# Kernel tuning notes

Hardware: AMD Instinct MI355X
Metric: run time of the kernel (lower is better)

The kernel has to match this reference:

```python
import jax, jax.numpy as jnp
import numpy as np

N_NODES = 50000
N_EDGES = 800000
IN_CH = 128
HID = 128


def setup_inputs() -> dict:
    key = jax.random.key(0)
    ks = jax.random.split(key, 16)
    inp = {
        "x": jax.random.normal(ks[0], (N_NODES, IN_CH), dtype=jnp.float32),
        "edge_index": jax.random.randint(ks[1], (2, N_EDGES), 0, N_NODES, dtype=jnp.int64),
        "batch_size": 1024,
    }
    dims = [(IN_CH, HID), (HID, HID), (HID, HID)]
    for i, (din, dout) in enumerate(dims):
        s = 1.0 / np.sqrt(din)
        inp[f"W_l{i}"] = jax.random.uniform(ks[2 + 4 * i], (dout, din), jnp.float32, -s, s)
        inp[f"b_l{i}"] = jax.random.uniform(ks[3 + 4 * i], (dout,), jnp.float32, -s, s)
        inp[f"W_r{i}"] = jax.random.uniform(ks[4 + 4 * i], (dout, din), jnp.float32, -s, s)
        inp[f"a{i}"] = jnp.full((dout,), 0.25, dtype=jnp.float32)  # PReLU slope
    return inp


def _sage_prelu(x, src, dst, W_l, b_l, W_r, a):
    # mean aggregation of source messages at target nodes
    msg_sum = jax.ops.segment_sum(x[src], dst, num_segments=N_NODES)  # [N, din]
    deg = jax.ops.segment_sum(jnp.ones((src.shape[0],), x.dtype), dst, num_segments=N_NODES)
    agg = msg_sum / jnp.maximum(deg, 1.0)[:, None]
    out = agg @ W_l.T + b_l + x @ W_r.T  # lin_l(aggr) + lin_r(x), bias on lin_l only
    return jnp.where(out > 0, out, a * out)  # per-channel PReLU


def reference(x, edge_index, batch_size, W_l0, b_l0, W_r0, a0, W_l1, b_l1, W_r1, a1, W_l2, b_l2, W_r2, a2):
    src, dst = edge_index[0], edge_index[1]
    x = _sage_prelu(x, src, dst, W_l0, b_l0, W_r0, a0)
    x = _sage_prelu(x, src, dst, W_l1, b_l1, W_r1, a1)
    x = _sage_prelu(x, src, dst, W_l2, b_l2, W_r2, a2)
    return x[:batch_size]
```

## Files before the change

kernel.cpp:

```cpp
#include <hip/hip_runtime.h>

#define NN 50000
#define NE 800000
#define C 128
#define SCAN_BLOCKS ((NN + 255) / 256)
#define ASTRIDE 136

typedef __attribute__((ext_vector_type(8))) short bf16x8;
typedef __attribute__((ext_vector_type(4))) float f32x4;
typedef unsigned short ushort;

__device__ inline ushort bf16_rn(float f) {
    unsigned u = __builtin_bit_cast(unsigned, f);
    u += 0x7FFF + ((u >> 16) & 1);
    return (ushort)(u >> 16);
}
__device__ inline void split_bf16(float f, ushort& hi, ushort& lo) {
    hi = bf16_rn(f);
    float hif = __builtin_bit_cast(float, (unsigned)hi << 16);
    lo = bf16_rn(f - hif);
}
__device__ inline float bf_lo(unsigned u) { return __builtin_bit_cast(float, u << 16); }
__device__ inline float bf_hi(unsigned u) { return __builtin_bit_cast(float, u & 0xFFFF0000u); }


__global__ __launch_bounds__(256)
void count_pos_kernel(const int* __restrict__ dst, int* __restrict__ deg,
                      int* __restrict__ pos, int n_edges) {
    int e0 = (blockIdx.x * 256 + threadIdx.x) * 8;
    if (e0 >= n_edges) return;
    int4 a = *(const int4*)(dst + e0);
    int4 b = *(const int4*)(dst + e0 + 4);
    int p0 = atomicAdd(&deg[a.x], 1);
    int p1 = atomicAdd(&deg[a.y], 1);
    int p2 = atomicAdd(&deg[a.z], 1);
    int p3 = atomicAdd(&deg[a.w], 1);
    int p4 = atomicAdd(&deg[b.x], 1);
    int p5 = atomicAdd(&deg[b.y], 1);
    int p6 = atomicAdd(&deg[b.z], 1);
    int p7 = atomicAdd(&deg[b.w], 1);
    *(int4*)(pos + e0)     = make_int4(p0, p1, p2, p3);
    *(int4*)(pos + e0 + 4) = make_int4(p4, p5, p6, p7);
}

__global__ __launch_bounds__(256)
void scan1_kernel(const int* __restrict__ deg, int* __restrict__ row_ptr,
                  int* __restrict__ bsum, int n) {
    __shared__ int wsum[4];
    __shared__ int wpre[4];
    int t = threadIdx.x, lane = t & 63, w = t >> 6;
    int i = blockIdx.x * 256 + t;
    int v = (i < n) ? deg[i] : 0;
    int s = v;
    #pragma unroll
    for (int off = 1; off < 64; off <<= 1) {
        int y = __shfl_up(s, off, 64);
        if (lane >= off) s += y;
    }
    if (lane == 63) wsum[w] = s;
    __syncthreads();
    if (t == 0) {
        int acc = 0;
        #pragma unroll
        for (int j = 0; j < 4; ++j) { wpre[j] = acc; acc += wsum[j]; }
        bsum[blockIdx.x] = acc;
    }
    __syncthreads();
    if (i < n) row_ptr[i] = wpre[w] + (s - v);
}

__global__ __launch_bounds__(256)
void scan2_kernel(const int* __restrict__ bsum, int* __restrict__ boff,
                  int* __restrict__ row_ptr, int nb, int n) {
    __shared__ int wsum[4];
    __shared__ int wpre[4];
    int t = threadIdx.x, lane = t & 63, w = t >> 6;
    int v = (t < nb) ? bsum[t] : 0;
    int s = v;
    #pragma unroll
    for (int off = 1; off < 64; off <<= 1) {
        int y = __shfl_up(s, off, 64);
        if (lane >= off) s += y;
    }
    if (lane == 63) wsum[w] = s;
    __syncthreads();
    if (t == 0) {
        int acc = 0;
        #pragma unroll
        for (int j = 0; j < 4; ++j) { wpre[j] = acc; acc += wsum[j]; }
        row_ptr[n] = acc;
    }
    __syncthreads();
    if (t < nb) boff[t] = wpre[w] + (s - v);
}

__global__ __launch_bounds__(256)
void scan3_kernel(int* __restrict__ row_ptr, const int* __restrict__ boff, int n) {
    int i = blockIdx.x * 256 + threadIdx.x;
    if (i < n) row_ptr[i] += boff[blockIdx.x];
}


__global__ __launch_bounds__(256)
void fill2_kernel(const int* __restrict__ src, const int* __restrict__ dst,
                  const int* __restrict__ row_ptr, const int* __restrict__ pos,
                  int* __restrict__ col, int n_edges) {
    int e0 = (blockIdx.x * 256 + threadIdx.x) * 8;
    if (e0 >= n_edges) return;
    int4 da = *(const int4*)(dst + e0);
    int4 db = *(const int4*)(dst + e0 + 4);
    int4 sa = *(const int4*)(src + e0);
    int4 sb = *(const int4*)(src + e0 + 4);
    int4 pa = *(const int4*)(pos + e0);
    int4 pb = *(const int4*)(pos + e0 + 4);
    col[row_ptr[da.x] + pa.x] = sa.x;
    col[row_ptr[da.y] + pa.y] = sa.y;
    col[row_ptr[da.z] + pa.z] = sa.z;
    col[row_ptr[da.w] + pa.w] = sa.w;
    col[row_ptr[db.x] + pb.x] = sb.x;
    col[row_ptr[db.y] + pb.y] = sb.y;
    col[row_ptr[db.z] + pb.z] = sb.z;
    col[row_ptr[db.w] + pb.w] = sb.w;
}


__global__ __launch_bounds__(256)
void split_kernel(const float* __restrict__ in, ushort* __restrict__ h,
                  ushort* __restrict__ l, int n4) {
    int i = blockIdx.x * 256 + threadIdx.x;
    if (i >= n4) return;
    f32x4 v = ((const f32x4*)in)[i];
    ushort h0, h1, h2, h3, l0, l1, l2, l3;
    split_bf16(v.x, h0, l0);
    split_bf16(v.y, h1, l1);
    split_bf16(v.z, h2, l2);
    split_bf16(v.w, h3, l3);
    *(uint2*)(h + i * 4) = make_uint2((unsigned)h0 | ((unsigned)h1 << 16),
                                      (unsigned)h2 | ((unsigned)h3 << 16));
    *(uint2*)(l + i * 4) = make_uint2((unsigned)l0 | ((unsigned)l1 << 16),
                                      (unsigned)l2 | ((unsigned)l3 << 16));
}


__global__ __launch_bounds__(256)
void agg_kernel(const ushort* __restrict__ xh, const int* __restrict__ row_ptr,
                const int* __restrict__ col, float* __restrict__ agg, int nodes) {
    int node = (blockIdx.x * blockDim.x + threadIdx.x) >> 6;
    int lane = threadIdx.x & 63;
    if (node >= nodes) return;
    int quad = lane >> 4;
    int ql   = lane & 15;
    int start = row_ptr[node], end = row_ptr[node + 1];
    const uint4* xr = (const uint4*)xh;
    float a0=0,a1=0,a2=0,a3=0,a4=0,a5=0,a6=0,a7=0;
    int e = start;
    for (; e + 7 < end; e += 8) {
        int i0 = col[e + quad];
        int i1 = col[e + 4 + quad];
        uint4 u0 = xr[(size_t)i0 * 16 + ql];
        uint4 u1 = xr[(size_t)i1 * 16 + ql];
        a0 += bf_lo(u0.x) + bf_lo(u1.x); a1 += bf_hi(u0.x) + bf_hi(u1.x);
        a2 += bf_lo(u0.y) + bf_lo(u1.y); a3 += bf_hi(u0.y) + bf_hi(u1.y);
        a4 += bf_lo(u0.z) + bf_lo(u1.z); a5 += bf_hi(u0.z) + bf_hi(u1.z);
        a6 += bf_lo(u0.w) + bf_lo(u1.w); a7 += bf_hi(u0.w) + bf_hi(u1.w);
    }
    for (; e + 3 < end; e += 4) {
        uint4 u = xr[(size_t)col[e + quad] * 16 + ql];
        a0 += bf_lo(u.x); a1 += bf_hi(u.x);
        a2 += bf_lo(u.y); a3 += bf_hi(u.y);
        a4 += bf_lo(u.z); a5 += bf_hi(u.z);
        a6 += bf_lo(u.w); a7 += bf_hi(u.w);
    }
    int rem = end - e;
    if (quad < rem) {
        uint4 u = xr[(size_t)col[e + quad] * 16 + ql];
        a0 += bf_lo(u.x); a1 += bf_hi(u.x);
        a2 += bf_lo(u.y); a3 += bf_hi(u.y);
        a4 += bf_lo(u.z); a5 += bf_hi(u.z);
        a6 += bf_lo(u.w); a7 += bf_hi(u.w);
    }
    a0 += __shfl_xor(a0, 16, 64); a0 += __shfl_xor(a0, 32, 64);
    a1 += __shfl_xor(a1, 16, 64); a1 += __shfl_xor(a1, 32, 64);
    a2 += __shfl_xor(a2, 16, 64); a2 += __shfl_xor(a2, 32, 64);
    a3 += __shfl_xor(a3, 16, 64); a3 += __shfl_xor(a3, 32, 64);
    a4 += __shfl_xor(a4, 16, 64); a4 += __shfl_xor(a4, 32, 64);
    a5 += __shfl_xor(a5, 16, 64); a5 += __shfl_xor(a5, 32, 64);
    a6 += __shfl_xor(a6, 16, 64); a6 += __shfl_xor(a6, 32, 64);
    a7 += __shfl_xor(a7, 16, 64); a7 += __shfl_xor(a7, 32, 64);
    if (quad == 0) {
        float inv = 1.0f / (float)max(end - start, 1);
        float* dst = agg + (size_t)node * C + ql * 8;
        *(f32x4*)dst       = (f32x4){a0 * inv, a1 * inv, a2 * inv, a3 * inv};
        *(f32x4*)(dst + 4) = (f32x4){a4 * inv, a5 * inv, a6 * inv, a7 * inv};
    }
}


__global__ __launch_bounds__(256, 3)
void gemm_kernel(const float* __restrict__ Ain,
                 const ushort* __restrict__ Xh, const ushort* __restrict__ Xl,
                 const float* __restrict__ Wl, const float* __restrict__ bl,
                 const float* __restrict__ Wr, const float* __restrict__ slope,
                 float* __restrict__ outf, ushort* __restrict__ outh,
                 ushort* __restrict__ outl, int rows) {
    __shared__ ushort Ahi[64 * ASTRIDE];
    __shared__ ushort Alo[64 * ASTRIDE];
    int t = threadIdx.x;
    int lane = t & 63;
    int w = t >> 6;
    int l = lane & 15;
    int q = lane >> 4;
    int row0 = blockIdx.x * 64;

    f32x4 acc[4][2];
    #pragma unroll
    for (int mt = 0; mt < 4; ++mt)
        #pragma unroll
        for (int nt = 0; nt < 2; ++nt)
            acc[mt][nt] = (f32x4){0.f, 0.f, 0.f, 0.f};

    #pragma unroll
    for (int mat = 0; mat < 2; ++mat) {
        const float* W = mat ? Wr : Wl;

        bf16x8 bhi[2][4], blo[2][4];
        #pragma unroll
        for (int nt = 0; nt < 2; ++nt) {
            int n = w * 32 + nt * 16 + l;
            const float* wp = W + n * C + q * 8;
            #pragma unroll
            for (int kb = 0; kb < 4; ++kb) {
                f32x4 w0 = *(const f32x4*)(wp + kb * 32);
                f32x4 w1 = *(const f32x4*)(wp + kb * 32 + 4);
                float f[8] = {w0.x, w0.y, w0.z, w0.w, w1.x, w1.y, w1.z, w1.w};
                bf16x8 h, o;
                #pragma unroll
                for (int j = 0; j < 8; ++j) {
                    ushort hh, ll;
                    split_bf16(f[j], hh, ll);
                    h[j] = (short)hh;
                    o[j] = (short)ll;
                }
                bhi[nt][kb] = h;
                blo[nt][kb] = o;
            }
        }

        __syncthreads();
        int ar = t >> 2;
        int aq = t & 3;
        int r = min(row0 + ar, rows - 1);
        ushort* dh = Ahi + ar * ASTRIDE + aq * 32;
        ushort* dl = Alo + ar * ASTRIDE + aq * 32;
        if (mat == 0) {
            const float* ap = Ain + (size_t)r * C + aq * 32;
            #pragma unroll
            for (int i = 0; i < 8; ++i) {
                f32x4 v = *(const f32x4*)(ap + i * 4);
                ushort h0, h1, h2, h3, l0, l1, l2, l3;
                split_bf16(v.x, h0, l0);
                split_bf16(v.y, h1, l1);
                split_bf16(v.z, h2, l2);
                split_bf16(v.w, h3, l3);
                *(uint2*)(dh + i * 4) = make_uint2((unsigned)h0 | ((unsigned)h1 << 16),
                                                   (unsigned)h2 | ((unsigned)h3 << 16));
                *(uint2*)(dl + i * 4) = make_uint2((unsigned)l0 | ((unsigned)l1 << 16),
                                                   (unsigned)l2 | ((unsigned)l3 << 16));
            }
        } else {
            const ushort* ph = Xh + (size_t)r * C + aq * 32;
            const ushort* pl = Xl + (size_t)r * C + aq * 32;
            #pragma unroll
            for (int i = 0; i < 4; ++i) {
                *(uint4*)(dh + i * 8) = *(const uint4*)(ph + i * 8);
                *(uint4*)(dl + i * 8) = *(const uint4*)(pl + i * 8);
            }
        }
        __syncthreads();

        #pragma unroll
        for (int kb = 0; kb < 4; ++kb) {
            #pragma unroll
            for (int mt = 0; mt < 4; ++mt) {
                int off = (mt * 16 + l) * ASTRIDE + kb * 32 + q * 8;
                bf16x8 ahi = *(const bf16x8*)(Ahi + off);
                bf16x8 alo = *(const bf16x8*)(Alo + off);
                #pragma unroll
                for (int nt = 0; nt < 2; ++nt) {
                    acc[mt][nt] = __builtin_amdgcn_mfma_f32_16x16x32_bf16(ahi, bhi[nt][kb], acc[mt][nt], 0, 0, 0);
                    acc[mt][nt] = __builtin_amdgcn_mfma_f32_16x16x32_bf16(alo, bhi[nt][kb], acc[mt][nt], 0, 0, 0);
                    acc[mt][nt] = __builtin_amdgcn_mfma_f32_16x16x32_bf16(ahi, blo[nt][kb], acc[mt][nt], 0, 0, 0);
                }
            }
        }
    }

    #pragma unroll
    for (int nt = 0; nt < 2; ++nt) {
        int n = w * 32 + nt * 16 + l;
        float b = bl[n], s = slope[n];
        #pragma unroll
        for (int mt = 0; mt < 4; ++mt) {
            #pragma unroll
            for (int rg = 0; rg < 4; ++rg) {
                int r = row0 + mt * 16 + q * 4 + rg;
                if (r < rows) {
                    float v = acc[mt][nt][rg] + b;
                    v = v > 0.f ? v : s * v;
                    if (outf) {
                        outf[(size_t)r * C + n] = v;
                    } else {
                        ushort hh, ll;
                        split_bf16(v, hh, ll);
                        outh[(size_t)r * C + n] = hh;
                        outl[(size_t)r * C + n] = ll;
                    }
                }
            }
        }
    }
}


extern "C" void kernel_launch(void* const* d_in, const int* in_sizes, int n_in,
                              void* d_out, int out_size, void* d_ws, size_t ws_size,
                              hipStream_t stream) {
    const float* x   = (const float*)d_in[0];
    const int*   src = (const int*)d_in[1];
    const int*   dst = src + NE;
    const float* Wl[3] = {(const float*)d_in[3], (const float*)d_in[7],  (const float*)d_in[11]};
    const float* bl[3] = {(const float*)d_in[4], (const float*)d_in[8],  (const float*)d_in[12]};
    const float* Wr[3] = {(const float*)d_in[5], (const float*)d_in[9],  (const float*)d_in[13]};
    const float* sl[3] = {(const float*)d_in[6], (const float*)d_in[10], (const float*)d_in[14]};

    int*   deg     = (int*)d_ws;
    int*   row_ptr = deg + 50016;
    int*   col     = row_ptr + 50016;
    int*   pos     = col + 800000;
    int*   bsum    = pos + 800000;
    int*   boff    = bsum + 256;
    float* agg     = (float*)(boff + 256);
    ushort* Ah     = (ushort*)(agg + (size_t)NN * C);
    ushort* Al     = Ah + (size_t)NN * C;
    ushort* Bh     = Al + (size_t)NN * C;
    ushort* Bl     = Bh + (size_t)NN * C;

    hipMemsetAsync(deg, 0, 50016 * sizeof(int), stream);

    const int E8B = (NE / 8 + 255) / 256;
    count_pos_kernel<<<E8B, 256, 0, stream>>>(dst, deg, pos, NE);
    scan1_kernel<<<SCAN_BLOCKS, 256, 0, stream>>>(deg, row_ptr, bsum, NN);
    scan2_kernel<<<1, 256, 0, stream>>>(bsum, boff, row_ptr, SCAN_BLOCKS, NN);
    scan3_kernel<<<SCAN_BLOCKS, 256, 0, stream>>>(row_ptr, boff, NN);
    fill2_kernel<<<E8B, 256, 0, stream>>>(src, dst, row_ptr, pos, col, NE);

    split_kernel<<<(NN * C / 4 + 255) / 256, 256, 0, stream>>>(x, Ah, Al, NN * C / 4);

    int rows_out = out_size / C;

    agg_kernel<<<(NN + 3) / 4, 256, 0, stream>>>(Ah, row_ptr, col, agg, NN);
    gemm_kernel<<<(NN + 63) / 64, 256, 0, stream>>>(agg, Ah, Al, Wl[0], bl[0], Wr[0], sl[0],
                                                    nullptr, Bh, Bl, NN);

    agg_kernel<<<(NN + 3) / 4, 256, 0, stream>>>(Bh, row_ptr, col, agg, NN);
    gemm_kernel<<<(NN + 63) / 64, 256, 0, stream>>>(agg, Bh, Bl, Wl[1], bl[1], Wr[1], sl[1],
                                                    nullptr, Ah, Al, NN);

    agg_kernel<<<(rows_out + 3) / 4, 256, 0, stream>>>(Ah, row_ptr, col, agg, rows_out);
    gemm_kernel<<<(rows_out + 63) / 64, 256, 0, stream>>>(agg, Ah, Al, Wl[2], bl[2], Wr[2], sl[2],
                                                          (float*)d_out, nullptr, nullptr, rows_out);
}
```

Before: 310.5 us.

## Fuse CSR build and bf16 split into one cooperative kernel with grid syncs

Replaces the memset, count, three scan, fill and split kernel launches with a single cooperative kernel that separates phases with grid-wide syncs. The bf16 hi/lo split of x is folded into the degree-counting phase as a grid-stride loop. This is meant to remove per-launch overhead and inter-kernel gaps for the small preprocessing steps. In exchange it adds grid.sync costs, and it depends on all 391 blocks being co-resident, which the cooperative launch requires.

```diff
diff --git a/kernel.cpp b/kernel.cpp
--- a/kernel.cpp
+++ b/kernel.cpp
@@ -1,9 +1,13 @@
 #include <hip/hip_runtime.h>
+#include <hip/hip_cooperative_groups.h>
+
+namespace cg = cooperative_groups;
 
 #define NN 50000
 #define NE 800000
 #define C 128
 #define SCAN_BLOCKS ((NN + 255) / 256)
+#define PRE_BLOCKS (NE / (256 * 8))
 #define ASTRIDE 136
 
 typedef __attribute__((ext_vector_type(8))) short bf16x8;
@@ -25,120 +29,121 @@
 
 
 __global__ __launch_bounds__(256)
-void count_pos_kernel(const int* __restrict__ dst, int* __restrict__ deg,
-                      int* __restrict__ pos, int n_edges) {
-    int e0 = (blockIdx.x * 256 + threadIdx.x) * 8;
-    if (e0 >= n_edges) return;
-    int4 a = *(const int4*)(dst + e0);
-    int4 b = *(const int4*)(dst + e0 + 4);
-    int p0 = atomicAdd(&deg[a.x], 1);
-    int p1 = atomicAdd(&deg[a.y], 1);
-    int p2 = atomicAdd(&deg[a.z], 1);
-    int p3 = atomicAdd(&deg[a.w], 1);
-    int p4 = atomicAdd(&deg[b.x], 1);
-    int p5 = atomicAdd(&deg[b.y], 1);
-    int p6 = atomicAdd(&deg[b.z], 1);
-    int p7 = atomicAdd(&deg[b.w], 1);
-    *(int4*)(pos + e0)     = make_int4(p0, p1, p2, p3);
-    *(int4*)(pos + e0 + 4) = make_int4(p4, p5, p6, p7);
-}
-
-__global__ __launch_bounds__(256)
-void scan1_kernel(const int* __restrict__ deg, int* __restrict__ row_ptr,
-                  int* __restrict__ bsum, int n) {
+void preproc_kernel(const int* __restrict__ src, const int* __restrict__ dst,
+                    const float* __restrict__ x,
+                    int* __restrict__ deg, int* __restrict__ row_ptr,
+                    int* __restrict__ pos, int* __restrict__ col,
+                    int* __restrict__ bsum, int* __restrict__ boff,
+                    ushort* __restrict__ Ah, ushort* __restrict__ Al) {
+    cg::grid_group grid = cg::this_grid();
     __shared__ int wsum[4];
     __shared__ int wpre[4];
     int t = threadIdx.x, lane = t & 63, w = t >> 6;
-    int i = blockIdx.x * 256 + t;
-    int v = (i < n) ? deg[i] : 0;
-    int s = v;
-    #pragma unroll
-    for (int off = 1; off < 64; off <<= 1) {
-        int y = __shfl_up(s, off, 64);
-        if (lane >= off) s += y;
-    }
-    if (lane == 63) wsum[w] = s;
-    __syncthreads();
-    if (t == 0) {
-        int acc = 0;
-        #pragma unroll
-        for (int j = 0; j < 4; ++j) { wpre[j] = acc; acc += wsum[j]; }
-        bsum[blockIdx.x] = acc;
-    }
-    __syncthreads();
-    if (i < n) row_ptr[i] = wpre[w] + (s - v);
-}
-
-__global__ __launch_bounds__(256)
-void scan2_kernel(const int* __restrict__ bsum, int* __restrict__ boff,
-                  int* __restrict__ row_ptr, int nb, int n) {
-    __shared__ int wsum[4];
-    __shared__ int wpre[4];
-    int t = threadIdx.x, lane = t & 63, w = t >> 6;
-    int v = (t < nb) ? bsum[t] : 0;
-    int s = v;
-    #pragma unroll
-    for (int off = 1; off < 64; off <<= 1) {
-        int y = __shfl_up(s, off, 64);
-        if (lane >= off) s += y;
-    }
-    if (lane == 63) wsum[w] = s;
-    __syncthreads();
-    if (t == 0) {
-        int acc = 0;
-        #pragma unroll
-        for (int j = 0; j < 4; ++j) { wpre[j] = acc; acc += wsum[j]; }
-        row_ptr[n] = acc;
-    }
-    __syncthreads();
-    if (t < nb) boff[t] = wpre[w] + (s - v);
-}
-
-__global__ __launch_bounds__(256)
-void scan3_kernel(int* __restrict__ row_ptr, const int* __restrict__ boff, int n) {
-    int i = blockIdx.x * 256 + threadIdx.x;
-    if (i < n) row_ptr[i] += boff[blockIdx.x];
-}
-
-
-__global__ __launch_bounds__(256)
-void fill2_kernel(const int* __restrict__ src, const int* __restrict__ dst,
-                  const int* __restrict__ row_ptr, const int* __restrict__ pos,
-                  int* __restrict__ col, int n_edges) {
-    int e0 = (blockIdx.x * 256 + threadIdx.x) * 8;
-    if (e0 >= n_edges) return;
-    int4 da = *(const int4*)(dst + e0);
-    int4 db = *(const int4*)(dst + e0 + 4);
-    int4 sa = *(const int4*)(src + e0);
-    int4 sb = *(const int4*)(src + e0 + 4);
-    int4 pa = *(const int4*)(pos + e0);
-    int4 pb = *(const int4*)(pos + e0 + 4);
-    col[row_ptr[da.x] + pa.x] = sa.x;
-    col[row_ptr[da.y] + pa.y] = sa.y;
-    col[row_ptr[da.z] + pa.z] = sa.z;
-    col[row_ptr[da.w] + pa.w] = sa.w;
-    col[row_ptr[db.x] + pb.x] = sb.x;
-    col[row_ptr[db.y] + pb.y] = sb.y;
-    col[row_ptr[db.z] + pb.z] = sb.z;
-    col[row_ptr[db.w] + pb.w] = sb.w;
-}
-
-
-__global__ __launch_bounds__(256)
-void split_kernel(const float* __restrict__ in, ushort* __restrict__ h,
-                  ushort* __restrict__ l, int n4) {
-    int i = blockIdx.x * 256 + threadIdx.x;
-    if (i >= n4) return;
-    f32x4 v = ((const f32x4*)in)[i];
-    ushort h0, h1, h2, h3, l0, l1, l2, l3;
-    split_bf16(v.x, h0, l0);
-    split_bf16(v.y, h1, l1);
-    split_bf16(v.z, h2, l2);
-    split_bf16(v.w, h3, l3);
-    *(uint2*)(h + i * 4) = make_uint2((unsigned)h0 | ((unsigned)h1 << 16),
-                                      (unsigned)h2 | ((unsigned)h3 << 16));
-    *(uint2*)(l + i * 4) = make_uint2((unsigned)l0 | ((unsigned)l1 << 16),
-                                      (unsigned)l2 | ((unsigned)l3 << 16));
+    int gid = blockIdx.x * 256 + t;
+    int nthreads = gridDim.x * 256;
+
+    for (int i = gid; i < NN; i += nthreads) deg[i] = 0;
+    grid.sync();
+
+    {
+        int e0 = gid * 8;
+        if (e0 < NE) {
+            int4 a = *(const int4*)(dst + e0);
+            int4 b = *(const int4*)(dst + e0 + 4);
+            int p0 = atomicAdd(&deg[a.x], 1);
+            int p1 = atomicAdd(&deg[a.y], 1);
+            int p2 = atomicAdd(&deg[a.z], 1);
+            int p3 = atomicAdd(&deg[a.w], 1);
+            int p4 = atomicAdd(&deg[b.x], 1);
+            int p5 = atomicAdd(&deg[b.y], 1);
+            int p6 = atomicAdd(&deg[b.z], 1);
+            int p7 = atomicAdd(&deg[b.w], 1);
+            *(int4*)(pos + e0)     = make_int4(p0, p1, p2, p3);
+            *(int4*)(pos + e0 + 4) = make_int4(p4, p5, p6, p7);
+        }
+        for (int i = gid; i < NN * C / 4; i += nthreads) {
+            f32x4 v = ((const f32x4*)x)[i];
+            ushort h0, h1, h2, h3, l0, l1, l2, l3;
+            split_bf16(v.x, h0, l0);
+            split_bf16(v.y, h1, l1);
+            split_bf16(v.z, h2, l2);
+            split_bf16(v.w, h3, l3);
+            *(uint2*)(Ah + (size_t)i * 4) = make_uint2((unsigned)h0 | ((unsigned)h1 << 16),
+                                                       (unsigned)h2 | ((unsigned)h3 << 16));
+            *(uint2*)(Al + (size_t)i * 4) = make_uint2((unsigned)l0 | ((unsigned)l1 << 16),
+                                                       (unsigned)l2 | ((unsigned)l3 << 16));
+        }
+    }
+    grid.sync();
+
+    if (blockIdx.x < SCAN_BLOCKS) {
+        int i = blockIdx.x * 256 + t;
+        int v = (i < NN) ? deg[i] : 0;
+        int s = v;
+        #pragma unroll
+        for (int off = 1; off < 64; off <<= 1) {
+            int y = __shfl_up(s, off, 64);
+            if (lane >= off) s += y;
+        }
+        if (lane == 63) wsum[w] = s;
+        __syncthreads();
+        if (t == 0) {
+            int acc = 0;
+            #pragma unroll
+            for (int j = 0; j < 4; ++j) { wpre[j] = acc; acc += wsum[j]; }
+            bsum[blockIdx.x] = acc;
+        }
+        __syncthreads();
+        if (i < NN) row_ptr[i] = wpre[w] + (s - v);
+    }
+    grid.sync();
+
+    if (blockIdx.x == 0) {
+        int v = (t < SCAN_BLOCKS) ? bsum[t] : 0;
+        int s = v;
+        #pragma unroll
+        for (int off = 1; off < 64; off <<= 1) {
+            int y = __shfl_up(s, off, 64);
+            if (lane >= off) s += y;
+        }
+        if (lane == 63) wsum[w] = s;
+        __syncthreads();
+        if (t == 0) {
+            int acc = 0;
+            #pragma unroll
+            for (int j = 0; j < 4; ++j) { wpre[j] = acc; acc += wsum[j]; }
+            row_ptr[NN] = acc;
+        }
+        __syncthreads();
+        if (t < SCAN_BLOCKS) boff[t] = wpre[w] + (s - v);
+    }
+    grid.sync();
+
+    if (blockIdx.x < SCAN_BLOCKS) {
+        int i = blockIdx.x * 256 + t;
+        if (i < NN) row_ptr[i] += boff[blockIdx.x];
+    }
+    grid.sync();
+
+    {
+        int e0 = gid * 8;
+        if (e0 < NE) {
+            int4 da = *(const int4*)(dst + e0);
+            int4 db = *(const int4*)(dst + e0 + 4);
+            int4 sa = *(const int4*)(src + e0);
+            int4 sb = *(const int4*)(src + e0 + 4);
+            int4 pa = *(const int4*)(pos + e0);
+            int4 pb = *(const int4*)(pos + e0 + 4);
+            col[row_ptr[da.x] + pa.x] = sa.x;
+            col[row_ptr[da.y] + pa.y] = sa.y;
+            col[row_ptr[da.z] + pa.z] = sa.z;
+            col[row_ptr[da.w] + pa.w] = sa.w;
+            col[row_ptr[db.x] + pb.x] = sb.x;
+            col[row_ptr[db.y] + pb.y] = sb.y;
+            col[row_ptr[db.z] + pb.z] = sb.z;
+            col[row_ptr[db.w] + pb.w] = sb.w;
+        }
+    }
 }
 
 
@@ -345,16 +350,14 @@
     ushort* Bh     = Al + (size_t)NN * C;
     ushort* Bl     = Bh + (size_t)NN * C;
 
-    hipMemsetAsync(deg, 0, 50016 * sizeof(int), stream);
-
-    const int E8B = (NE / 8 + 255) / 256;
-    count_pos_kernel<<<E8B, 256, 0, stream>>>(dst, deg, pos, NE);
-    scan1_kernel<<<SCAN_BLOCKS, 256, 0, stream>>>(deg, row_ptr, bsum, NN);
-    scan2_kernel<<<1, 256, 0, stream>>>(bsum, boff, row_ptr, SCAN_BLOCKS, NN);
-    scan3_kernel<<<SCAN_BLOCKS, 256, 0, stream>>>(row_ptr, boff, NN);
-    fill2_kernel<<<E8B, 256, 0, stream>>>(src, dst, row_ptr, pos, col, NE);
-
-    split_kernel<<<(NN * C / 4 + 255) / 256, 256, 0, stream>>>(x, Ah, Al, NN * C / 4);
+    {
+        void* args[] = {(void*)&src, (void*)&dst, (void*)&x,
+                        (void*)&deg, (void*)&row_ptr, (void*)&pos, (void*)&col,
+                        (void*)&bsum, (void*)&boff, (void*)&Ah, (void*)&Al};
+        hipLaunchCooperativeKernel((const void*)preproc_kernel,
+                                   dim3((NE / 8 + 255) / 256), dim3(256),
+                                   args, 0, stream);
+    }
 
     int rows_out = out_size / C;
 
```

Result: slower. 536.4 us (+72.7%).

## Fuse degree count with input split, drop scan3, emit bf16 split from aggregation

Applied to the files above, without the earlier changes.

Merges the edge-count atomics and the fp32-to-bf16 hi/lo split of x into one launch, using separate block ranges for each. Removes the third scan pass by adding the block offset at every row_ptr use in fill and aggregation. The aggregation kernel now writes the mean directly as bf16 hi/lo pairs, so the GEMM loads pre-split operands uniformly instead of converting fp32 in its staging loop. This cuts kernel launches and GEMM staging work, at the cost of extra boff lookups per edge and per node.

```diff
diff --git a/kernel.cpp b/kernel.cpp
--- a/kernel.cpp
+++ b/kernel.cpp
@@ -4,6 +4,8 @@
 #define NE 800000
 #define C 128
 #define SCAN_BLOCKS ((NN + 255) / 256)
+#define E8B ((NE / 8 + 255) / 256)
+#define SPLITB 1563
 #define ASTRIDE 136
 
 typedef __attribute__((ext_vector_type(8))) short bf16x8;
@@ -25,32 +27,52 @@
 
 
 __global__ __launch_bounds__(256)
-void count_pos_kernel(const int* __restrict__ dst, int* __restrict__ deg,
-                      int* __restrict__ pos, int n_edges) {
-    int e0 = (blockIdx.x * 256 + threadIdx.x) * 8;
-    if (e0 >= n_edges) return;
-    int4 a = *(const int4*)(dst + e0);
-    int4 b = *(const int4*)(dst + e0 + 4);
-    int p0 = atomicAdd(&deg[a.x], 1);
-    int p1 = atomicAdd(&deg[a.y], 1);
-    int p2 = atomicAdd(&deg[a.z], 1);
-    int p3 = atomicAdd(&deg[a.w], 1);
-    int p4 = atomicAdd(&deg[b.x], 1);
-    int p5 = atomicAdd(&deg[b.y], 1);
-    int p6 = atomicAdd(&deg[b.z], 1);
-    int p7 = atomicAdd(&deg[b.w], 1);
-    *(int4*)(pos + e0)     = make_int4(p0, p1, p2, p3);
-    *(int4*)(pos + e0 + 4) = make_int4(p4, p5, p6, p7);
-}
+void count_split_kernel(const int* __restrict__ dst, const float* __restrict__ x,
+                        int* __restrict__ deg, int* __restrict__ pos,
+                        ushort* __restrict__ Ah, ushort* __restrict__ Al) {
+    int t = threadIdx.x;
+    if (blockIdx.x < E8B) {
+        int e0 = (blockIdx.x * 256 + t) * 8;
+        if (e0 >= NE) return;
+        int4 a = *(const int4*)(dst + e0);
+        int4 b = *(const int4*)(dst + e0 + 4);
+        int p0 = atomicAdd(&deg[a.x], 1);
+        int p1 = atomicAdd(&deg[a.y], 1);
+        int p2 = atomicAdd(&deg[a.z], 1);
+        int p3 = atomicAdd(&deg[a.w], 1);
+        int p4 = atomicAdd(&deg[b.x], 1);
+        int p5 = atomicAdd(&deg[b.y], 1);
+        int p6 = atomicAdd(&deg[b.z], 1);
+        int p7 = atomicAdd(&deg[b.w], 1);
+        *(int4*)(pos + e0)     = make_int4(p0, p1, p2, p3);
+        *(int4*)(pos + e0 + 4) = make_int4(p4, p5, p6, p7);
+    } else {
+        int tid = (blockIdx.x - E8B) * 256 + t;
+        const int total = NN * C / 4;
+        for (int i = tid; i < total; i += SPLITB * 256) {
+            f32x4 v = ((const f32x4*)x)[i];
+            ushort h0, h1, h2, h3, l0, l1, l2, l3;
+            split_bf16(v.x, h0, l0);
+            split_bf16(v.y, h1, l1);
+            split_bf16(v.z, h2, l2);
+            split_bf16(v.w, h3, l3);
+            *(uint2*)(Ah + (size_t)i * 4) = make_uint2((unsigned)h0 | ((unsigned)h1 << 16),
+                                                       (unsigned)h2 | ((unsigned)h3 << 16));
+            *(uint2*)(Al + (size_t)i * 4) = make_uint2((unsigned)l0 | ((unsigned)l1 << 16),
+                                                       (unsigned)l2 | ((unsigned)l3 << 16));
+        }
+    }
+}
+
 
 __global__ __launch_bounds__(256)
 void scan1_kernel(const int* __restrict__ deg, int* __restrict__ row_ptr,
-                  int* __restrict__ bsum, int n) {
+                  int* __restrict__ bsum) {
     __shared__ int wsum[4];
     __shared__ int wpre[4];
     int t = threadIdx.x, lane = t & 63, w = t >> 6;
     int i = blockIdx.x * 256 + t;
-    int v = (i < n) ? deg[i] : 0;
+    int v = (i < NN) ? deg[i] : 0;
     int s = v;
     #pragma unroll
     for (int off = 1; off < 64; off <<= 1) {
@@ -66,16 +88,16 @@
         bsum[blockIdx.x] = acc;
     }
     __syncthreads();
-    if (i < n) row_ptr[i] = wpre[w] + (s - v);
-}
-
-__global__ __launch_bounds__(256)
-void scan2_kernel(const int* __restrict__ bsum, int* __restrict__ boff,
-                  int* __restrict__ row_ptr, int nb, int n) {
+    if (i <= NN) row_ptr[i] = wpre[w] + (s - v);
+}
+
+
+__global__ __launch_bounds__(256)
+void scan2_kernel(const int* __restrict__ bsum, int* __restrict__ boff) {
     __shared__ int wsum[4];
     __shared__ int wpre[4];
     int t = threadIdx.x, lane = t & 63, w = t >> 6;
-    int v = (t < nb) ? bsum[t] : 0;
+    int v = (t < SCAN_BLOCKS) ? bsum[t] : 0;
     int s = v;
     #pragma unroll
     for (int off = 1; off < 64; off <<= 1) {
@@ -88,69 +110,46 @@
         int acc = 0;
         #pragma unroll
         for (int j = 0; j < 4; ++j) { wpre[j] = acc; acc += wsum[j]; }
-        row_ptr[n] = acc;
     }
     __syncthreads();
-    if (t < nb) boff[t] = wpre[w] + (s - v);
-}
-
-__global__ __launch_bounds__(256)
-void scan3_kernel(int* __restrict__ row_ptr, const int* __restrict__ boff, int n) {
-    int i = blockIdx.x * 256 + threadIdx.x;
-    if (i < n) row_ptr[i] += boff[blockIdx.x];
+    if (t < SCAN_BLOCKS) boff[t] = wpre[w] + (s - v);
 }
 
 
 __global__ __launch_bounds__(256)
 void fill2_kernel(const int* __restrict__ src, const int* __restrict__ dst,
-                  const int* __restrict__ row_ptr, const int* __restrict__ pos,
-                  int* __restrict__ col, int n_edges) {
+                  const int* __restrict__ row_ptr, const int* __restrict__ boff,
+                  const int* __restrict__ pos, int* __restrict__ col) {
     int e0 = (blockIdx.x * 256 + threadIdx.x) * 8;
-    if (e0 >= n_edges) return;
+    if (e0 >= NE) return;
     int4 da = *(const int4*)(dst + e0);
     int4 db = *(const int4*)(dst + e0 + 4);
     int4 sa = *(const int4*)(src + e0);
     int4 sb = *(const int4*)(src + e0 + 4);
     int4 pa = *(const int4*)(pos + e0);
     int4 pb = *(const int4*)(pos + e0 + 4);
-    col[row_ptr[da.x] + pa.x] = sa.x;
-    col[row_ptr[da.y] + pa.y] = sa.y;
-    col[row_ptr[da.z] + pa.z] = sa.z;
-    col[row_ptr[da.w] + pa.w] = sa.w;
-    col[row_ptr[db.x] + pb.x] = sb.x;
-    col[row_ptr[db.y] + pb.y] = sb.y;
-    col[row_ptr[db.z] + pb.z] = sb.z;
-    col[row_ptr[db.w] + pb.w] = sb.w;
-}
-
-
-__global__ __launch_bounds__(256)
-void split_kernel(const float* __restrict__ in, ushort* __restrict__ h,
-                  ushort* __restrict__ l, int n4) {
-    int i = blockIdx.x * 256 + threadIdx.x;
-    if (i >= n4) return;
-    f32x4 v = ((const f32x4*)in)[i];
-    ushort h0, h1, h2, h3, l0, l1, l2, l3;
-    split_bf16(v.x, h0, l0);
-    split_bf16(v.y, h1, l1);
-    split_bf16(v.z, h2, l2);
-    split_bf16(v.w, h3, l3);
-    *(uint2*)(h + i * 4) = make_uint2((unsigned)h0 | ((unsigned)h1 << 16),
-                                      (unsigned)h2 | ((unsigned)h3 << 16));
-    *(uint2*)(l + i * 4) = make_uint2((unsigned)l0 | ((unsigned)l1 << 16),
-                                      (unsigned)l2 | ((unsigned)l3 << 16));
+    col[row_ptr[da.x] + boff[da.x >> 8] + pa.x] = sa.x;
+    col[row_ptr[da.y] + boff[da.y >> 8] + pa.y] = sa.y;
+    col[row_ptr[da.z] + boff[da.z >> 8] + pa.z] = sa.z;
+    col[row_ptr[da.w] + boff[da.w >> 8] + pa.w] = sa.w;
+    col[row_ptr[db.x] + boff[db.x >> 8] + pb.x] = sb.x;
+    col[row_ptr[db.y] + boff[db.y >> 8] + pb.y] = sb.y;
+    col[row_ptr[db.z] + boff[db.z >> 8] + pb.z] = sb.z;
+    col[row_ptr[db.w] + boff[db.w >> 8] + pb.w] = sb.w;
 }
 
 
 __global__ __launch_bounds__(256)
 void agg_kernel(const ushort* __restrict__ xh, const int* __restrict__ row_ptr,
-                const int* __restrict__ col, float* __restrict__ agg, int nodes) {
+                const int* __restrict__ boff, const int* __restrict__ col,
+                ushort* __restrict__ aggh, ushort* __restrict__ aggl, int nodes) {
     int node = (blockIdx.x * blockDim.x + threadIdx.x) >> 6;
     int lane = threadIdx.x & 63;
     if (node >= nodes) return;
     int quad = lane >> 4;
     int ql   = lane & 15;
-    int start = row_ptr[node], end = row_ptr[node + 1];
+    int start = row_ptr[node] + boff[node >> 8];
+    int end   = row_ptr[node + 1] + boff[(node + 1) >> 8];
     const uint4* xr = (const uint4*)xh;
     float a0=0,a1=0,a2=0,a3=0,a4=0,a5=0,a6=0,a7=0;
     int e = start;
@@ -189,15 +188,25 @@
     a7 += __shfl_xor(a7, 16, 64); a7 += __shfl_xor(a7, 32, 64);
     if (quad == 0) {
         float inv = 1.0f / (float)max(end - start, 1);
-        float* dst = agg + (size_t)node * C + ql * 8;
-        *(f32x4*)dst       = (f32x4){a0 * inv, a1 * inv, a2 * inv, a3 * inv};
-        *(f32x4*)(dst + 4) = (f32x4){a4 * inv, a5 * inv, a6 * inv, a7 * inv};
+        float m[8] = {a0*inv, a1*inv, a2*inv, a3*inv, a4*inv, a5*inv, a6*inv, a7*inv};
+        ushort h[8], o[8];
+        #pragma unroll
+        for (int j = 0; j < 8; ++j) split_bf16(m[j], h[j], o[j]);
+        size_t off = (size_t)node * C + ql * 8;
+        *(uint4*)(aggh + off) = make_uint4((unsigned)h[0] | ((unsigned)h[1] << 16),
+                                           (unsigned)h[2] | ((unsigned)h[3] << 16),
+                                           (unsigned)h[4] | ((unsigned)h[5] << 16),
+                                           (unsigned)h[6] | ((unsigned)h[7] << 16));
+        *(uint4*)(aggl + off) = make_uint4((unsigned)o[0] | ((unsigned)o[1] << 16),
+                                           (unsigned)o[2] | ((unsigned)o[3] << 16),
+                                           (unsigned)o[4] | ((unsigned)o[5] << 16),
+                                           (unsigned)o[6] | ((unsigned)o[7] << 16));
     }
 }
 
 
 __global__ __launch_bounds__(256, 3)
-void gemm_kernel(const float* __restrict__ Ain,
+void gemm_kernel(const ushort* __restrict__ Ah, const ushort* __restrict__ Al,
                  const ushort* __restrict__ Xh, const ushort* __restrict__ Xl,
                  const float* __restrict__ Wl, const float* __restrict__ bl,
                  const float* __restrict__ Wr, const float* __restrict__ slope,
@@ -222,6 +231,8 @@
     #pragma unroll
     for (int mat = 0; mat < 2; ++mat) {
         const float* W = mat ? Wr : Wl;
+        const ushort* Ph = mat ? Xh : Ah;
+        const ushort* Pl = mat ? Xl : Al;
 
         bf16x8 bhi[2][4], blo[2][4];
         #pragma unroll
@@ -252,29 +263,12 @@
         int r = min(row0 + ar, rows - 1);
         ushort* dh = Ahi + ar * ASTRIDE + aq * 32;
         ushort* dl = Alo + ar * ASTRIDE + aq * 32;
-        if (mat == 0) {
-            const float* ap = Ain + (size_t)r * C + aq * 32;
-            #pragma unroll
-            for (int i = 0; i < 8; ++i) {
-                f32x4 v = *(const f32x4*)(ap + i * 4);
-                ushort h0, h1, h2, h3, l0, l1, l2, l3;
-                split_bf16(v.x, h0, l0);
-                split_bf16(v.y, h1, l1);
-                split_bf16(v.z, h2, l2);
-                split_bf16(v.w, h3, l3);
-                *(uint2*)(dh + i * 4) = make_uint2((unsigned)h0 | ((unsigned)h1 << 16),
-                                                   (unsigned)h2 | ((unsigned)h3 << 16));
-                *(uint2*)(dl + i * 4) = make_uint2((unsigned)l0 | ((unsigned)l1 << 16),
-                                                   (unsigned)l2 | ((unsigned)l3 << 16));
-            }
-        } else {
-            const ushort* ph = Xh + (size_t)r * C + aq * 32;
-            const ushort* pl = Xl + (size_t)r * C + aq * 32;
-            #pragma unroll
-            for (int i = 0; i < 4; ++i) {
-                *(uint4*)(dh + i * 8) = *(const uint4*)(ph + i * 8);
-                *(uint4*)(dl + i * 8) = *(const uint4*)(pl + i * 8);
-            }
+        const ushort* ph = Ph + (size_t)r * C + aq * 32;
+        const ushort* pl = Pl + (size_t)r * C + aq * 32;
+        #pragma unroll
+        for (int i = 0; i < 4; ++i) {
+            *(uint4*)(dh + i * 8) = *(const uint4*)(ph + i * 8);
+            *(uint4*)(dl + i * 8) = *(const uint4*)(pl + i * 8);
         }
         __syncthreads();
 
@@ -339,34 +333,31 @@
     int*   pos     = col + 800000;
     int*   bsum    = pos + 800000;
     int*   boff    = bsum + 256;
-    float* agg     = (float*)(boff + 256);
-    ushort* Ah     = (ushort*)(agg + (size_t)NN * C);
+    ushort* Gh     = (ushort*)(boff + 256);
+    ushort* Gl     = Gh + (size_t)NN * C;
+    ushort* Ah     = Gl + (size_t)NN * C;
     ushort* Al     = Ah + (size_t)NN * C;
     ushort* Bh     = Al + (size_t)NN * C;
     ushort* Bl     = Bh + (size_t)NN * C;
 
     hipMemsetAsync(deg, 0, 50016 * sizeof(int), stream);
 
-    const int E8B = (NE / 8 + 255) / 256;
-    count_pos_kernel<<<E8B, 256, 0, stream>>>(dst, deg, pos, NE);
-    scan1_kernel<<<SCAN_BLOCKS, 256, 0, stream>>>(deg, row_ptr, bsum, NN);
-    scan2_kernel<<<1, 256, 0, stream>>>(bsum, boff, row_ptr, SCAN_BLOCKS, NN);
-    scan3_kernel<<<SCAN_BLOCKS, 256, 0, stream>>>(row_ptr, boff, NN);
-    fill2_kernel<<<E8B, 256, 0, stream>>>(src, dst, row_ptr, pos, col, NE);
-
-    split_kernel<<<(NN * C / 4 + 255) / 256, 256, 0, stream>>>(x, Ah, Al, NN * C / 4);
+    count_split_kernel<<<E8B + SPLITB, 256, 0, stream>>>(dst, x, deg, pos, Ah, Al);
+    scan1_kernel<<<SCAN_BLOCKS, 256, 0, stream>>>(deg, row_ptr, bsum);
+    scan2_kernel<<<1, 256, 0, stream>>>(bsum, boff);
+    fill2_kernel<<<E8B, 256, 0, stream>>>(src, dst, row_ptr, boff, pos, col);
 
     int rows_out = out_size / C;
 
-    agg_kernel<<<(NN + 3) / 4, 256, 0, stream>>>(Ah, row_ptr, col, agg, NN);
-    gemm_kernel<<<(NN + 63) / 64, 256, 0, stream>>>(agg, Ah, Al, Wl[0], bl[0], Wr[0], sl[0],
+    agg_kernel<<<(NN + 3) / 4, 256, 0, stream>>>(Ah, row_ptr, boff, col, Gh, Gl, NN);
+    gemm_kernel<<<(NN + 63) / 64, 256, 0, stream>>>(Gh, Gl, Ah, Al, Wl[0], bl[0], Wr[0], sl[0],
                                                     nullptr, Bh, Bl, NN);
 
-    agg_kernel<<<(NN + 3) / 4, 256, 0, stream>>>(Bh, row_ptr, col, agg, NN);
-    gemm_kernel<<<(NN + 63) / 64, 256, 0, stream>>>(agg, Bh, Bl, Wl[1], bl[1], Wr[1], sl[1],
+    agg_kernel<<<(NN + 3) / 4, 256, 0, stream>>>(Bh, row_ptr, boff, col, Gh, Gl, NN);
+    gemm_kernel<<<(NN + 63) / 64, 256, 0, stream>>>(Gh, Gl, Bh, Bl, Wl[1], bl[1], Wr[1], sl[1],
                                                     nullptr, Ah, Al, NN);
 
-    agg_kernel<<<(rows_out + 3) / 4, 256, 0, stream>>>(Ah, row_ptr, col, agg, rows_out);
-    gemm_kernel<<<(rows_out + 63) / 64, 256, 0, stream>>>(agg, Ah, Al, Wl[2], bl[2], Wr[2], sl[2],
+    agg_kernel<<<(rows_out + 3) / 4, 256, 0, stream>>>(Ah, row_ptr, boff, col, Gh, Gl, rows_out);
+    gemm_kernel<<<(rows_out + 63) / 64, 256, 0, stream>>>(Gh, Gl, Ah, Al, Wl[2], bl[2], Wr[2], sl[2],
                                                           (float*)d_out, nullptr, nullptr, rows_out);
 }
```

After: 312.2 us. No clear change (+0.5%).
